# Kernel tuning notes

Measured on AMD Instinct MI355X. Metric: run time of the kernel, lower is better.

## Reference

```python
import jax, jax.numpy as jnp
import numpy as np

TEMPERATURE = 0.6


def setup_inputs() -> dict:
    key = jax.random.key(0)
    k1, k2, k3 = jax.random.split(key, 3)
    B, IN, OUT, C = 8192, 256, 32, 50
    x = jax.random.uniform(k1, (B, IN), dtype=jnp.float32)
    weight = jax.random.normal(k2, (C, OUT, IN), dtype=jnp.float32) * 0.05
    bias = jax.random.normal(k3, (C, 1, OUT), dtype=jnp.float32) * 0.05
    return {"x": x, "weight": weight, "bias": bias}


def reference(x, weight, bias):
    # gamma[c,i] = L1 norm of weight over out dim: sum_o |W[c,o,i]|
    gamma = jnp.sum(jnp.abs(weight), axis=1)            # [C, IN]
    alpha = jax.nn.softmax(gamma / TEMPERATURE, axis=1)  # [C, IN]
    alpha_norm = alpha / jnp.max(alpha, axis=1, keepdims=True)  # [C, IN]
    # gated input per class: [C, B, IN]
    xg = x[None, :, :] * alpha_norm[:, None, :]
    # per-class GEMM: y[c,b,o] = sum_i xg[c,b,i] * W[c,o,i]
    y = jnp.einsum('cbi,coi->cbo', xg, weight) + bias    # [C, B, OUT]
    return jnp.transpose(y, (1, 0, 2))                   # [B, C, OUT]
```

## Files before the change

kernel.cpp:

```cpp
#include <hip/hip_runtime.h>
#include <hip/hip_bf16.h>

typedef __bf16 bf16x8 __attribute__((ext_vector_type(8)));
typedef float  f32x4  __attribute__((ext_vector_type(4)));

#define B_ROWS 8192
#define IN_DIM 256
#define OUT_DIM 32
#define NCLS 50
#define INV_T (1.0f / 0.6f)

#define CVT_BLOCKS 1024
#define GGRID 1024
#define NGRP 13
#define OSTRIDE (NCLS * OUT_DIM)

__device__ __forceinline__ void gload_lds16(const void* g, void* l) {
    __builtin_amdgcn_global_load_lds(
        (const __attribute__((address_space(1))) void*)g,
        (__attribute__((address_space(3))) void*)l, 16, 0, 0);
}

__global__ __launch_bounds__(256) void prep(const float* __restrict__ x,
                                            const float* __restrict__ w,
                                            __bf16* __restrict__ xb,
                                            __bf16* __restrict__ wb) {
    __shared__ float wm[4];
    int bid = blockIdx.x;
    if (bid < NCLS) {
        int c = bid;
        int i = threadIdx.x;
        const float* wc = w + (size_t)c * OUT_DIM * IN_DIM + i;
        float wv[OUT_DIM];
#pragma unroll
        for (int o = 0; o < OUT_DIM; ++o) wv[o] = wc[o * IN_DIM];
        float gsum = 0.f;
#pragma unroll
        for (int o = 0; o < OUT_DIM; ++o) gsum += fabsf(wv[o]);
        float m = gsum;
#pragma unroll
        for (int s = 1; s < 64; s <<= 1) m = fmaxf(m, __shfl_xor(m, s));
        if ((threadIdx.x & 63) == 0) wm[threadIdx.x >> 6] = m;
        __syncthreads();
        m = fmaxf(fmaxf(wm[0], wm[1]), fmaxf(wm[2], wm[3]));
        float an = __expf((gsum - m) * INV_T);
        __bf16* wo = wb + (size_t)c * OUT_DIM * IN_DIM + i;
#pragma unroll
        for (int o = 0; o < OUT_DIM; ++o)
            wo[o * IN_DIM] = (__bf16)(wv[o] * an);
    } else {
        int i = ((bid - NCLS) * 256 + threadIdx.x) * 8;
        float4 v0 = *reinterpret_cast<const float4*>(x + i);
        float4 v1 = *reinterpret_cast<const float4*>(x + i + 4);
        bf16x8 r;
        r[0] = (__bf16)v0.x; r[1] = (__bf16)v0.y; r[2] = (__bf16)v0.z; r[3] = (__bf16)v0.w;
        r[4] = (__bf16)v1.x; r[5] = (__bf16)v1.y; r[6] = (__bf16)v1.z; r[7] = (__bf16)v1.w;
        *reinterpret_cast<bf16x8*>(xb + i) = r;
    }
}

__global__ __launch_bounds__(256, 4) void gemm(const __bf16* __restrict__ xb,
                                               const __bf16* __restrict__ wb,
                                               const float* __restrict__ bias,
                                               float* __restrict__ out) {
    __shared__ __align__(16) char lds[4 * 8192];

    int bid = blockIdx.x;
    int cg = (bid * NGRP) >> 10;
    int first = (cg * GGRID + NGRP - 1) / NGRP;
    int next  = ((cg + 1) * GGRID + NGRP - 1) / NGRP;
    int j = bid - first;
    int np = next - first;
    int u0 = (j * 512) / np;
    int u1 = ((j + 1) * 512) / np;
    int nch = u1 - u0;

    int lane = threadIdx.x & 63;
    int w4 = threadIdx.x >> 6;
    int c = cg * 4 + ((cg == NGRP - 1) ? (w4 & 1) : w4);
    int l15 = lane & 15;
    int g = lane >> 4;
    int s31 = lane & 31;
    int lr = lane >> 5;

    const __bf16* wp = wb + ((size_t)c * OUT_DIM + l15) * IN_DIM + g * 8;
    bf16x8 W[16];
#pragma unroll
    for (int kk = 0; kk < 8; ++kk) {
        W[kk]     = *reinterpret_cast<const bf16x8*>(wp + kk * 32);
        W[8 + kk] = *reinterpret_cast<const bf16x8*>(wp + 16 * IN_DIM + kk * 32);
    }
    f32x4 bv0 = *reinterpret_cast<const f32x4*>(bias + c * OUT_DIM + g * 4);
    f32x4 bv1 = *reinterpret_cast<const f32x4*>(bias + c * OUT_DIM + 16 + g * 4);
#pragma unroll
    for (int kk = 0; kk < 16; ++kk)
        asm volatile("" : "+v"(W[kk]));
    asm volatile("" : "+v"(bv0), "+v"(bv1));
    asm volatile("s_waitcnt vmcnt(0)" ::: "memory");
    __builtin_amdgcn_sched_barrier(0);

    const char* arows = (const char*)xb + (size_t)u0 * 16 * 512;

#define STAGE(BUF, CH)                                                            \
    _Pragma("unroll") for (int i2 = 0; i2 < 2; ++i2) {                            \
        int re = w4 * 4 + 2 * i2;                                                 \
        int r = re + lr;                                                          \
        gload_lds16(arows + (size_t)(CH) * 8192 + (size_t)r * 512 + ((s31 ^ r) * 16), \
                    (BUF) + re * 512);                                            \
    }
#define VMW(N) asm volatile("s_waitcnt vmcnt(" #N ")" ::: "memory")

    STAGE(lds, 0)
    STAGE(lds + 8192, 1)

    float* orow = out + (size_t)(u0 * 16 + l15) * OSTRIDE + c * OUT_DIM + g * 4;

    for (int k = 0; k < nch; ++k) {
        char* sb = lds + ((k + 2) & 3) * 8192;
        STAGE(sb, k + 2)
        if (k == 0)      VMW(4);
        else if (k == 1) VMW(6);
        else             VMW(8);
        __builtin_amdgcn_sched_barrier(0);
        __builtin_amdgcn_s_barrier();
        __builtin_amdgcn_sched_barrier(0);

        const char* cb = lds + (k & 3) * 8192;
        f32x4 acc0 = bv0;
        f32x4 acc1 = bv1;
#pragma unroll
        for (int kk = 0; kk < 8; ++kk) {
            bf16x8 a = *reinterpret_cast<const bf16x8*>(
                cb + (size_t)l15 * 512 + (((4 * kk + g) ^ l15) * 16));
            acc0 = __builtin_amdgcn_mfma_f32_16x16x32_bf16(W[kk],     a, acc0, 0, 0, 0);
            acc1 = __builtin_amdgcn_mfma_f32_16x16x32_bf16(W[8 + kk], a, acc1, 0, 0, 0);
        }
        float* op = orow + (size_t)k * 16 * OSTRIDE;
        *reinterpret_cast<f32x4*>(op) = acc0;
        *reinterpret_cast<f32x4*>(op + 16) = acc1;
    }
#undef STAGE
#undef VMW
}

extern "C" void kernel_launch(void* const* d_in, const int* in_sizes, int n_in,
                              void* d_out, int out_size, void* d_ws, size_t ws_size,
                              hipStream_t stream) {
    const float* x    = (const float*)d_in[0];
    const float* w    = (const float*)d_in[1];
    const float* bias = (const float*)d_in[2];
    float* out = (float*)d_out;

    __bf16* xb = (__bf16*)d_ws;
    __bf16* wb = xb + (size_t)B_ROWS * IN_DIM;

    prep<<<NCLS + CVT_BLOCKS, 256, 0, stream>>>(x, w, xb, wb);
    gemm<<<GGRID, 256, 0, stream>>>(xb, wb, bias, out);
}
```

Baseline: 34.43 us.

## Fuse x conversion into GEMM and stream weights through LDS per row block

The separate pass that converts x to bf16 is removed. Each GEMM block now loads its 32 rows of x in fp32, converts them in registers and keeps them resident, then streams all 50 classes' bf16 weights through an 8-slot LDS ring with bias cached in LDS. The work split changes from class-group by row-chunk to blocks of 32 rows covering all classes, using 256 blocks of 512 threads. This saves the xb write and re-read and a large prep grid, but every block must now reload the full weight set (about 800KB) from L2 and the grid is smaller.

Result: faster. 32.92 us (-4.4%).

```diff
diff --git a/kernel.cpp b/kernel.cpp
--- a/kernel.cpp
+++ b/kernel.cpp
@@ -4,15 +4,10 @@
 typedef __bf16 bf16x8 __attribute__((ext_vector_type(8)));
 typedef float  f32x4  __attribute__((ext_vector_type(4)));
 
-#define B_ROWS 8192
 #define IN_DIM 256
 #define OUT_DIM 32
 #define NCLS 50
 #define INV_T (1.0f / 0.6f)
-
-#define CVT_BLOCKS 1024
-#define GGRID 1024
-#define NGRP 13
 #define OSTRIDE (NCLS * OUT_DIM)
 
 __device__ __forceinline__ void gload_lds16(const void* g, void* l) {
@@ -21,125 +16,116 @@
         (__attribute__((address_space(3))) void*)l, 16, 0, 0);
 }
 
-__global__ __launch_bounds__(256) void prep(const float* __restrict__ x,
-                                            const float* __restrict__ w,
-                                            __bf16* __restrict__ xb,
-                                            __bf16* __restrict__ wb) {
+__global__ __launch_bounds__(256) void prep_w(const float* __restrict__ w,
+                                              __bf16* __restrict__ wb) {
     __shared__ float wm[4];
-    int bid = blockIdx.x;
-    if (bid < NCLS) {
-        int c = bid;
-        int i = threadIdx.x;
-        const float* wc = w + (size_t)c * OUT_DIM * IN_DIM + i;
-        float wv[OUT_DIM];
+    int c = blockIdx.x;
+    int i = threadIdx.x;
+    const float* wc = w + (size_t)c * OUT_DIM * IN_DIM + i;
+    float wv[OUT_DIM];
 #pragma unroll
-        for (int o = 0; o < OUT_DIM; ++o) wv[o] = wc[o * IN_DIM];
-        float gsum = 0.f;
+    for (int o = 0; o < OUT_DIM; ++o) wv[o] = wc[o * IN_DIM];
+    float gsum = 0.f;
 #pragma unroll
-        for (int o = 0; o < OUT_DIM; ++o) gsum += fabsf(wv[o]);
-        float m = gsum;
+    for (int o = 0; o < OUT_DIM; ++o) gsum += fabsf(wv[o]);
+    float m = gsum;
 #pragma unroll
-        for (int s = 1; s < 64; s <<= 1) m = fmaxf(m, __shfl_xor(m, s));
-        if ((threadIdx.x & 63) == 0) wm[threadIdx.x >> 6] = m;
-        __syncthreads();
-        m = fmaxf(fmaxf(wm[0], wm[1]), fmaxf(wm[2], wm[3]));
-        float an = __expf((gsum - m) * INV_T);
-        __bf16* wo = wb + (size_t)c * OUT_DIM * IN_DIM + i;
+    for (int s = 1; s < 64; s <<= 1) m = fmaxf(m, __shfl_xor(m, s));
+    if ((threadIdx.x & 63) == 0) wm[threadIdx.x >> 6] = m;
+    __syncthreads();
+    m = fmaxf(fmaxf(wm[0], wm[1]), fmaxf(wm[2], wm[3]));
+    float an = __expf((gsum - m) * INV_T);
+    __bf16* wo = wb + (size_t)c * OUT_DIM * IN_DIM + i;
 #pragma unroll
-        for (int o = 0; o < OUT_DIM; ++o)
-            wo[o * IN_DIM] = (__bf16)(wv[o] * an);
-    } else {
-        int i = ((bid - NCLS) * 256 + threadIdx.x) * 8;
-        float4 v0 = *reinterpret_cast<const float4*>(x + i);
-        float4 v1 = *reinterpret_cast<const float4*>(x + i + 4);
-        bf16x8 r;
-        r[0] = (__bf16)v0.x; r[1] = (__bf16)v0.y; r[2] = (__bf16)v0.z; r[3] = (__bf16)v0.w;
-        r[4] = (__bf16)v1.x; r[5] = (__bf16)v1.y; r[6] = (__bf16)v1.z; r[7] = (__bf16)v1.w;
-        *reinterpret_cast<bf16x8*>(xb + i) = r;
-    }
+    for (int o = 0; o < OUT_DIM; ++o)
+        wo[o * IN_DIM] = (__bf16)(wv[o] * an);
 }
 
-__global__ __launch_bounds__(256, 4) void gemm(const __bf16* __restrict__ xb,
+__global__ __launch_bounds__(512, 2) void gemm(const float* __restrict__ x,
                                                const __bf16* __restrict__ wb,
                                                const float* __restrict__ bias,
                                                float* __restrict__ out) {
-    __shared__ __align__(16) char lds[4 * 8192];
+    __shared__ __align__(16) char lds[8 * 16384 + 6400];
+    float* bias_lds = (float*)(lds + 8 * 16384);
 
     int bid = blockIdx.x;
-    int cg = (bid * NGRP) >> 10;
-    int first = (cg * GGRID + NGRP - 1) / NGRP;
-    int next  = ((cg + 1) * GGRID + NGRP - 1) / NGRP;
-    int j = bid - first;
-    int np = next - first;
-    int u0 = (j * 512) / np;
-    int u1 = ((j + 1) * 512) / np;
-    int nch = u1 - u0;
-
-    int lane = threadIdx.x & 63;
-    int w4 = threadIdx.x >> 6;
-    int c = cg * 4 + ((cg == NGRP - 1) ? (w4 & 1) : w4);
+    int row0 = bid * 32;
+    int tid = threadIdx.x;
+    int lane = tid & 63;
+    int w8 = tid >> 6;
+    int rg = w8 & 1;
+    int oh = (w8 >> 1) & 1;
+    int cpar = w8 >> 2;
     int l15 = lane & 15;
     int g = lane >> 4;
     int s31 = lane & 31;
     int lr = lane >> 5;
 
-    const __bf16* wp = wb + ((size_t)c * OUT_DIM + l15) * IN_DIM + g * 8;
-    bf16x8 W[16];
+    const float* xrow = x + (size_t)(row0 + rg * 16 + l15) * IN_DIM + g * 8;
+    bf16x8 A[8];
 #pragma unroll
     for (int kk = 0; kk < 8; ++kk) {
-        W[kk]     = *reinterpret_cast<const bf16x8*>(wp + kk * 32);
-        W[8 + kk] = *reinterpret_cast<const bf16x8*>(wp + 16 * IN_DIM + kk * 32);
+        f32x4 lo = *reinterpret_cast<const f32x4*>(xrow + kk * 32);
+        f32x4 hi = *reinterpret_cast<const f32x4*>(xrow + kk * 32 + 4);
+        bf16x8 a;
+        a[0] = (__bf16)lo[0]; a[1] = (__bf16)lo[1]; a[2] = (__bf16)lo[2]; a[3] = (__bf16)lo[3];
+        a[4] = (__bf16)hi[0]; a[5] = (__bf16)hi[1]; a[6] = (__bf16)hi[2]; a[7] = (__bf16)hi[3];
+        A[kk] = a;
     }
-    f32x4 bv0 = *reinterpret_cast<const f32x4*>(bias + c * OUT_DIM + g * 4);
-    f32x4 bv1 = *reinterpret_cast<const f32x4*>(bias + c * OUT_DIM + 16 + g * 4);
+
+    const char* wsrc = (const char*)wb;
 #pragma unroll
-    for (int kk = 0; kk < 16; ++kk)
-        asm volatile("" : "+v"(W[kk]));
-    asm volatile("" : "+v"(bv0), "+v"(bv1));
-    asm volatile("s_waitcnt vmcnt(0)" ::: "memory");
-    __builtin_amdgcn_sched_barrier(0);
+    for (int j = 0; j < 12; ++j) {
+        int re = w8 * 24 + 2 * j;
+        int rr = re + lr;
+        gload_lds16(wsrc + (size_t)rr * 512 + ((s31 ^ (rr & 15)) * 16),
+                    lds + re * 512);
+    }
+    if (tid < 400) {
+        f32x4 b = *reinterpret_cast<const f32x4*>(bias + tid * 4);
+        *reinterpret_cast<f32x4*>(bias_lds + tid * 4) = b;
+    }
+#pragma unroll
+    for (int kk = 0; kk < 8; ++kk)
+        asm volatile("" : "+v"(A[kk]));
+    __syncthreads();
 
-    const char* arows = (const char*)xb + (size_t)u0 * 16 * 512;
+    float* outp = out + (size_t)(row0 + rg * 16 + l15) * OSTRIDE
+                      + cpar * OUT_DIM + oh * 16 + g * 4;
 
-#define STAGE(BUF, CH)                                                            \
-    _Pragma("unroll") for (int i2 = 0; i2 < 2; ++i2) {                            \
-        int re = w4 * 4 + 2 * i2;                                                 \
-        int r = re + lr;                                                          \
-        gload_lds16(arows + (size_t)(CH) * 8192 + (size_t)r * 512 + ((s31 ^ r) * 16), \
-                    (BUF) + re * 512);                                            \
-    }
 #define VMW(N) asm volatile("s_waitcnt vmcnt(" #N ")" ::: "memory")
-
-    STAGE(lds, 0)
-    STAGE(lds + 8192, 1)
-
-    float* orow = out + (size_t)(u0 * 16 + l15) * OSTRIDE + c * OUT_DIM + g * 4;
-
-    for (int k = 0; k < nch; ++k) {
-        char* sb = lds + ((k + 2) & 3) * 8192;
-        STAGE(sb, k + 2)
-        if (k == 0)      VMW(4);
-        else if (k == 1) VMW(6);
-        else             VMW(8);
+#pragma unroll
+    for (int r = 0; r < 25; ++r) {
+        if (r <= 22)      VMW(11);
+        else if (r == 23) VMW(7);
+        else              VMW(3);
         __builtin_amdgcn_sched_barrier(0);
         __builtin_amdgcn_s_barrier();
         __builtin_amdgcn_sched_barrier(0);
 
-        const char* cb = lds + (k & 3) * 8192;
-        f32x4 acc0 = bv0;
-        f32x4 acc1 = bv1;
+        if (r <= 21) {
+            int cb = 2 * r + 6;
+#pragma unroll
+            for (int j = 0; j < 4; ++j) {
+                int re = w8 * 8 + 2 * j;
+                int rr = re + lr;
+                gload_lds16(wsrc + ((size_t)cb * 32 + rr) * 512 + ((s31 ^ (rr & 15)) * 16),
+                            lds + ((cb & 7) * 32 + re) * 512);
+            }
+        }
+
+        int c = 2 * r + cpar;
+        const char* slot = lds + (size_t)(c & 7) * 16384;
+        f32x4 acc = *reinterpret_cast<const f32x4*>(bias_lds + c * 32 + oh * 16 + g * 4);
 #pragma unroll
         for (int kk = 0; kk < 8; ++kk) {
-            bf16x8 a = *reinterpret_cast<const bf16x8*>(
-                cb + (size_t)l15 * 512 + (((4 * kk + g) ^ l15) * 16));
-            acc0 = __builtin_amdgcn_mfma_f32_16x16x32_bf16(W[kk],     a, acc0, 0, 0, 0);
-            acc1 = __builtin_amdgcn_mfma_f32_16x16x32_bf16(W[8 + kk], a, acc1, 0, 0, 0);
+            bf16x8 Wf = *reinterpret_cast<const bf16x8*>(
+                slot + (size_t)(oh * 16 + l15) * 512 + (((4 * kk + g) ^ l15) * 16));
+            acc = __builtin_amdgcn_mfma_f32_16x16x32_bf16(Wf, A[kk], acc, 0, 0, 0);
         }
-        float* op = orow + (size_t)k * 16 * OSTRIDE;
-        *reinterpret_cast<f32x4*>(op) = acc0;
-        *reinterpret_cast<f32x4*>(op + 16) = acc1;
+        *reinterpret_cast<f32x4*>(outp) = acc;
+        outp += 64;
     }
-#undef STAGE
 #undef VMW
 }
 
@@ -151,9 +137,8 @@
     const float* bias = (const float*)d_in[2];
     float* out = (float*)d_out;
 
-    __bf16* xb = (__bf16*)d_ws;
-    __bf16* wb = xb + (size_t)B_ROWS * IN_DIM;
+    __bf16* wb = (__bf16*)d_ws;
 
-    prep<<<NCLS + CVT_BLOCKS, 256, 0, stream>>>(x, w, xb, wb);
-    gemm<<<GGRID, 256, 0, stream>>>(xb, wb, bias, out);
+    prep_w<<<NCLS, 256, 0, stream>>>(w, wb);
+    gemm<<<256, 512, 0, stream>>>(x, wb, bias, out);
 }
```

## Assign one class per block with per-wave row tiles and LDS-staged weights

Applied to the files above, without the earlier changes.

Replaces the grouped-class grid, where four classes share each staged x chunk, with a grid of one class per block and 16 row tiles. Each wave streams its own 128 rows in half-K double-buffered stages. Weights are loaded into registers through LDS instead of directly from global memory, and the occupancy hint rises to 5 blocks per SM. This makes the schedule simpler and more uniform, but x is now re-read once per class, and each block writes only 128-byte output segments per row.

New measurement: 60.37 us. 75.3% more time.

```diff
diff --git a/kernel.cpp b/kernel.cpp
--- a/kernel.cpp
+++ b/kernel.cpp
@@ -11,8 +11,7 @@
 #define INV_T (1.0f / 0.6f)
 
 #define CVT_BLOCKS 1024
-#define GGRID 1024
-#define NGRP 13
+#define ROWTILES 16
 #define OSTRIDE (NCLS * OUT_DIM)
 
 __device__ __forceinline__ void gload_lds16(const void* g, void* l) {
@@ -59,88 +58,105 @@
     }
 }
 
-__global__ __launch_bounds__(256, 4) void gemm(const __bf16* __restrict__ xb,
+__global__ __launch_bounds__(256, 5) void gemm(const __bf16* __restrict__ xb,
                                                const __bf16* __restrict__ wb,
                                                const float* __restrict__ bias,
                                                float* __restrict__ out) {
     __shared__ __align__(16) char lds[4 * 8192];
 
     int bid = blockIdx.x;
-    int cg = (bid * NGRP) >> 10;
-    int first = (cg * GGRID + NGRP - 1) / NGRP;
-    int next  = ((cg + 1) * GGRID + NGRP - 1) / NGRP;
-    int j = bid - first;
-    int np = next - first;
-    int u0 = (j * 512) / np;
-    int u1 = ((j + 1) * 512) / np;
-    int nch = u1 - u0;
-
+    int c = bid >> 4;
+    int rt = bid & (ROWTILES - 1);
+    int row0 = rt * 512;
     int lane = threadIdx.x & 63;
     int w4 = threadIdx.x >> 6;
-    int c = cg * 4 + ((cg == NGRP - 1) ? (w4 & 1) : w4);
     int l15 = lane & 15;
     int g = lane >> 4;
     int s31 = lane & 31;
     int lr = lane >> 5;
+    int r4 = lane >> 4;
 
-    const __bf16* wp = wb + ((size_t)c * OUT_DIM + l15) * IN_DIM + g * 8;
+    char* buf0 = lds + w4 * 8192;
+    char* buf1 = buf0 + 4096;
+
+    const char* arows = (const char*)(xb + (size_t)(row0 + w4 * 128) * IN_DIM);
+
+#define STAGE_H(BUF, H)                                                            \
+    _Pragma("unroll") for (int j = 0; j < 4; ++j) {                                \
+        int rr = ((H) >> 1) * 16 + j * 4 + r4;                                     \
+        gload_lds16(arows + (size_t)rr * 512 + ((H) & 1) * 256                     \
+                        + ((l15 ^ (rr & 15)) * 16),                                \
+                    (BUF) + j * 1024);                                             \
+    }
+
+    STAGE_H(buf0, 0)
+
+    const char* wsrc = (const char*)(wb + (size_t)c * OUT_DIM * IN_DIM);
+#pragma unroll
+    for (int j = 0; j < 4; ++j) {
+        int re = w4 * 8 + 2 * j;
+        int r = re + lr;
+        gload_lds16(wsrc + (size_t)r * 512 + ((s31 ^ (r & 15)) * 16),
+                    lds + w4 * 8192 + 4096 + (re & 7) * 512);
+    }
+
+    asm volatile("s_waitcnt vmcnt(0)" ::: "memory");
+    __syncthreads();
+    __builtin_amdgcn_sched_barrier(0);
+
     bf16x8 W[16];
 #pragma unroll
     for (int kk = 0; kk < 8; ++kk) {
-        W[kk]     = *reinterpret_cast<const bf16x8*>(wp + kk * 32);
-        W[8 + kk] = *reinterpret_cast<const bf16x8*>(wp + 16 * IN_DIM + kk * 32);
+        int wr1 = l15;
+        int wr2 = 16 + l15;
+        W[kk]     = *reinterpret_cast<const bf16x8*>(
+            lds + (wr1 >> 3) * 8192 + 4096 + (wr1 & 7) * 512 + (((4 * kk + g) ^ l15) * 16));
+        W[8 + kk] = *reinterpret_cast<const bf16x8*>(
+            lds + (wr2 >> 3) * 8192 + 4096 + (wr2 & 7) * 512 + (((4 * kk + g) ^ l15) * 16));
     }
-    f32x4 bv0 = *reinterpret_cast<const f32x4*>(bias + c * OUT_DIM + g * 4);
-    f32x4 bv1 = *reinterpret_cast<const f32x4*>(bias + c * OUT_DIM + 16 + g * 4);
 #pragma unroll
     for (int kk = 0; kk < 16; ++kk)
         asm volatile("" : "+v"(W[kk]));
-    asm volatile("" : "+v"(bv0), "+v"(bv1));
-    asm volatile("s_waitcnt vmcnt(0)" ::: "memory");
     __builtin_amdgcn_sched_barrier(0);
+    __syncthreads();
 
-    const char* arows = (const char*)xb + (size_t)u0 * 16 * 512;
+    STAGE_H(buf1, 1)
 
-#define STAGE(BUF, CH)                                                            \
-    _Pragma("unroll") for (int i2 = 0; i2 < 2; ++i2) {                            \
-        int re = w4 * 4 + 2 * i2;                                                 \
-        int r = re + lr;                                                          \
-        gload_lds16(arows + (size_t)(CH) * 8192 + (size_t)r * 512 + ((s31 ^ r) * 16), \
-                    (BUF) + re * 512);                                            \
-    }
-#define VMW(N) asm volatile("s_waitcnt vmcnt(" #N ")" ::: "memory")
+    f32x4 bv0 = *reinterpret_cast<const f32x4*>(bias + c * OUT_DIM + g * 4);
+    f32x4 bv1 = *reinterpret_cast<const f32x4*>(bias + c * OUT_DIM + 16 + g * 4);
 
-    STAGE(lds, 0)
-    STAGE(lds + 8192, 1)
+    float* orow = out + (size_t)(row0 + w4 * 128 + l15) * OSTRIDE + c * OUT_DIM + g * 4;
 
-    float* orow = out + (size_t)(u0 * 16 + l15) * OSTRIDE + c * OUT_DIM + g * 4;
-
-    for (int k = 0; k < nch; ++k) {
-        char* sb = lds + ((k + 2) & 3) * 8192;
-        STAGE(sb, k + 2)
-        if (k == 0)      VMW(4);
-        else if (k == 1) VMW(6);
-        else             VMW(8);
-        __builtin_amdgcn_sched_barrier(0);
-        __builtin_amdgcn_s_barrier();
+    f32x4 acc0, acc1;
+#pragma unroll
+    for (int h = 0; h < 16; ++h) {
+        if (h >= 1 && h <= 14) {
+            char* nbuf = (h & 1) ? buf0 : buf1;
+            STAGE_H(nbuf, h + 1)
+        }
+        if (h == 0)           asm volatile("s_waitcnt vmcnt(4)" ::: "memory");
+        else if (h == 15)     asm volatile("s_waitcnt vmcnt(0)" ::: "memory");
+        else if (h & 1)       asm volatile("s_waitcnt vmcnt(4)" ::: "memory");
+        else                  asm volatile("s_waitcnt vmcnt(6)" ::: "memory");
         __builtin_amdgcn_sched_barrier(0);
 
-        const char* cb = lds + (k & 3) * 8192;
-        f32x4 acc0 = bv0;
-        f32x4 acc1 = bv1;
+        if (!(h & 1)) { acc0 = bv0; acc1 = bv1; }
+        const char* cb = (h & 1) ? buf1 : buf0;
+        int h4 = (h & 1) * 4;
 #pragma unroll
-        for (int kk = 0; kk < 8; ++kk) {
+        for (int kkl = 0; kkl < 4; ++kkl) {
             bf16x8 a = *reinterpret_cast<const bf16x8*>(
-                cb + (size_t)l15 * 512 + (((4 * kk + g) ^ l15) * 16));
-            acc0 = __builtin_amdgcn_mfma_f32_16x16x32_bf16(W[kk],     a, acc0, 0, 0, 0);
-            acc1 = __builtin_amdgcn_mfma_f32_16x16x32_bf16(W[8 + kk], a, acc1, 0, 0, 0);
+                cb + (size_t)l15 * 256 + (((4 * kkl + g) ^ l15) * 16));
+            acc0 = __builtin_amdgcn_mfma_f32_16x16x32_bf16(W[h4 + kkl],     a, acc0, 0, 0, 0);
+            acc1 = __builtin_amdgcn_mfma_f32_16x16x32_bf16(W[8 + h4 + kkl], a, acc1, 0, 0, 0);
         }
-        float* op = orow + (size_t)k * 16 * OSTRIDE;
-        *reinterpret_cast<f32x4*>(op) = acc0;
-        *reinterpret_cast<f32x4*>(op + 16) = acc1;
+        if (h & 1) {
+            float* op = orow + (size_t)(h >> 1) * 16 * OSTRIDE;
+            *reinterpret_cast<f32x4*>(op) = acc0;
+            *reinterpret_cast<f32x4*>(op + 16) = acc1;
+        }
     }
-#undef STAGE
-#undef VMW
+#undef STAGE_H
 }
 
 extern "C" void kernel_launch(void* const* d_in, const int* in_sizes, int n_in,
@@ -155,5 +171,5 @@
     __bf16* wb = xb + (size_t)B_ROWS * IN_DIM;
 
     prep<<<NCLS + CVT_BLOCKS, 256, 0, stream>>>(x, w, xb, wb);
-    gemm<<<GGRID, 256, 0, stream>>>(xb, wb, bias, out);
+    gemm<<<NCLS * ROWTILES, 256, 0, stream>>>(xb, wb, bias, out);
 }
```
